# Performance work log

Hardware: AMD Instinct MI355X
Metric: run time of the kernel (lower is better)

## Reference

```python
import jax, jax.numpy as jnp
import numpy as np

D_MODEL = 1024
D_STATE = 16
LN_EPS = 1e-5


def setup_inputs() -> dict:
    key = jax.random.key(0)
    ks = jax.random.split(key, 10)
    B, T = 8, 4096
    s = 1.0 / np.sqrt(D_MODEL)
    inp = {
        "x": jax.random.normal(ks[0], (B, T, D_MODEL), jnp.float32),
        "h0": jnp.zeros((B, D_STATE), jnp.float32),
        "mask": jnp.ones((B, T), jnp.float32),
        # params
        "A_diag": -jnp.abs(jax.random.normal(ks[1], (D_STATE,), jnp.float32) * 0.01),
        "W_delta": jax.random.uniform(ks[2], (D_STATE, D_MODEL), jnp.float32, -s, s),
        "W_B": jax.random.uniform(ks[3], (D_STATE, D_MODEL), jnp.float32, -s, s),
        "W_C": jax.random.uniform(ks[4], (D_STATE, D_MODEL), jnp.float32, -s, s),
        "W_out": jax.random.uniform(ks[5], (D_MODEL, D_STATE), jnp.float32, -1/np.sqrt(D_STATE), 1/np.sqrt(D_STATE)),
        "D": jnp.ones((D_MODEL,), jnp.float32),
        "W_gate": jax.random.uniform(ks[6], (D_MODEL, D_MODEL), jnp.float32, -s, s),
        "b_gate": jax.random.uniform(ks[7], (D_MODEL,), jnp.float32, -s, s),
        "ln_w": jnp.ones((D_MODEL,), jnp.float32),
        "ln_b": jnp.zeros((D_MODEL,), jnp.float32),
    }
    return inp


def _layernorm(x, w, b):
    mu = jnp.mean(x, axis=-1, keepdims=True)
    var = jnp.var(x, axis=-1, keepdims=True)
    return (x - mu) * jax.lax.rsqrt(var + LN_EPS) * w + b


def reference(x, h0, mask, A_diag, W_delta, W_B, W_C, W_out, D, W_gate, b_gate, ln_w, ln_b):
    # Per-step projections depend only on x_t -> vectorize over T up front.
    gate = jax.nn.sigmoid(_layernorm(jnp.einsum('btd,ed->bte', x, W_gate) + b_gate, ln_w, ln_b))
    xg = gate * x                                        # [B,T,d_model]
    delta = jax.nn.softplus(jnp.einsum('btd,sd->bts', xg, W_delta))
    Bt = jnp.einsum('btd,sd->bts', xg, W_B)              # [B,T,d_state]
    Ct = jnp.einsum('btd,sd->bts', xg, W_C)
    A_bar = jnp.exp(delta * A_diag)                      # [B,T,d_state]
    m = mask[..., None]                                  # [B,T,1]

    def step(h, inputs):
        a_t, b_t, m_t = inputs                           # [B,ds],[B,ds],[B,1]
        h_cand = jnp.tanh(a_t * h + b_t)
        h_new = h_cand * m_t + h * (1.0 - m_t)
        return h_new, h_new

    # scan over time: move T to leading axis
    h_final, hs = jax.lax.scan(
        step, h0,
        (jnp.swapaxes(A_bar, 0, 1), jnp.swapaxes(Bt, 0, 1), jnp.swapaxes(m, 0, 1)))
    hs = jnp.swapaxes(hs, 0, 1)                          # [B,T,d_state]
    s = Ct * hs
    y = jnp.einsum('bts,ds->btd', s, W_out) + D * x      # [B,T,d_model]
    return (y, h_final)
```

## Files before the change

### kernel.cpp

```cpp
#include <hip/hip_runtime.h>
#include <hip/hip_bf16.h>
#include <cstdint>

#define M_TOK   32768
#define LNEPS   1e-5f
#define TWO_LOG2E 2.8853900817779268f

typedef float  f32x4 __attribute__((ext_vector_type(4)));
typedef short  s16x8 __attribute__((ext_vector_type(8)));
typedef unsigned long long ull;

__device__ __forceinline__ unsigned short f2b(float v) {
  return __builtin_bit_cast(unsigned short, __float2bfloat16(v));
}
__device__ __forceinline__ float b2f(unsigned short u) {
  return __bfloat162float(__builtin_bit_cast(__hip_bfloat16, u));
}
__device__ __forceinline__ float red64(float v) {
#pragma unroll
  for (int off = 32; off >= 1; off >>= 1) v += __shfl_xor(v, off, 64);
  return v;
}

__device__ __forceinline__ void async_cp16(const void* g, void* l) {
  using gp = const __attribute__((address_space(1))) char*;
  using lp = __attribute__((address_space(3))) char*;
  __builtin_amdgcn_global_load_lds((gp)(uint64_t)g,
                                   (lp)(uint32_t)(uint64_t)l, 16, 0, 0);
}

__global__ __launch_bounds__(256) void k_convert(
    const float* __restrict__ x, const float* __restrict__ wg,
    const float* __restrict__ wd, const float* __restrict__ wb,
    const float* __restrict__ wc,
    unsigned short* __restrict__ Xb, unsigned short* __restrict__ Wgb,
    unsigned short* __restrict__ Wcat) {
  int i = blockIdx.x * 256 + threadIdx.x;
  const float* src;
  unsigned short* dst;
  if (i < 8388608) {
    src = x + (size_t)i * 4; dst = Xb + (size_t)i * 4;
  } else if (i < 8650752) {
    int j = i - 8388608;
    src = wg + (size_t)j * 4; dst = Wgb + (size_t)j * 4;
  } else {
    int j = i - 8650752;
    int e = j * 4;
    if (e < 16384)       src = wd + e;
    else if (e < 32768)  src = wb + (e - 16384);
    else                 src = wc + (e - 32768);
    dst = Wcat + e;
  }
  float4 v = *(const float4*)src;
  ushort4 o;
  o.x = f2b(v.x); o.y = f2b(v.y); o.z = f2b(v.z); o.w = f2b(v.w);
  *(ushort4*)dst = o;
}

__global__ __launch_bounds__(256, 2) void k_gemm_gate(
    const unsigned short* __restrict__ A,
    const unsigned short* __restrict__ Bm,
    unsigned short* __restrict__ C) {
  __shared__ unsigned short As[128 * 32];
  __shared__ unsigned short Bs[128 * 32];
  const int tid  = threadIdx.x;
  const int wave = tid >> 6, lane = tid & 63;
  const int wr = wave >> 1, wc = wave & 1;
  const int lrow = lane & 15, lq = lane >> 4;
  const int lin  = blockIdx.y * gridDim.x + blockIdx.x;
  const int unit = (lin & 7) * 256 + (lin >> 3);
  const int m0 = (unit >> 3) * 128;
  const int n0 = (unit & 7) * 128;
  const int crow  = tid >> 2;
  const int ccol  = (tid & 3) * 8;

  f32x4 acc[4][4];
#pragma unroll
  for (int i = 0; i < 4; i++)
#pragma unroll
    for (int j = 0; j < 4; j++) acc[i][j] = (f32x4){0.f, 0.f, 0.f, 0.f};

  for (int k0 = 0; k0 < 1024; k0 += 32) {
    async_cp16(A + (size_t)(m0 + crow) * 1024 + k0 + ccol,
               (void*)(As + (wave * 64) * 8));
    async_cp16(A + (size_t)(m0 + crow + 64) * 1024 + k0 + ccol,
               (void*)(As + (256 + wave * 64) * 8));
    async_cp16(Bm + (size_t)(n0 + crow) * 1024 + k0 + ccol,
               (void*)(Bs + (wave * 64) * 8));
    async_cp16(Bm + (size_t)(n0 + crow + 64) * 1024 + k0 + ccol,
               (void*)(Bs + (256 + wave * 64) * 8));
    __syncthreads();

    s16x8 af[4], bfr[4];
#pragma unroll
    for (int i = 0; i < 4; i++)
      af[i] = *(const s16x8*)(As + (wr * 64 + i * 16 + lrow) * 32 + lq * 8);
#pragma unroll
    for (int j = 0; j < 4; j++)
      bfr[j] = *(const s16x8*)(Bs + (wc * 64 + j * 16 + lrow) * 32 + lq * 8);
#pragma unroll
    for (int i = 0; i < 4; i++)
#pragma unroll
      for (int j = 0; j < 4; j++)
        acc[i][j] = __builtin_amdgcn_mfma_f32_16x16x32_bf16(
            af[i], bfr[j], acc[i][j], 0, 0, 0);
    __syncthreads();
  }

#pragma unroll
  for (int i = 0; i < 4; i++)
#pragma unroll
    for (int j = 0; j < 4; j++)
#pragma unroll
      for (int r = 0; r < 4; r++) {
        int row = m0 + wr * 64 + i * 16 + lq * 4 + r;
        int col = n0 + wc * 64 + j * 16 + lrow;
        C[(size_t)row * 1024 + col] = f2b(acc[i][j][r]);
      }
}

__global__ __launch_bounds__(256) void k_lnproj(
    const unsigned short* __restrict__ G,
    const float* __restrict__ x,
    const float* __restrict__ bgp, const float* __restrict__ lnw,
    const float* __restrict__ lnb,
    const unsigned short* __restrict__ Wcat,
    const float* __restrict__ A_diag,
    float* __restrict__ UV, float* __restrict__ Ct, int* __restrict__ flags) {
  __shared__ unsigned short As[64 * 32];
  __shared__ unsigned short Bs[48 * 32];
  __shared__ float muL[64], rsL[64];
  const int tid  = threadIdx.x;
  const int wave = tid >> 6, lane = tid & 63;
  const int lrow = lane & 15, lq = lane >> 4;
  const int r0 = blockIdx.x * 64;
  const int crow = tid >> 2, ccol = (tid & 3) * 8;

  if (blockIdx.x == 0 && tid < 8)
    __hip_atomic_store(&flags[tid], 0, __ATOMIC_RELAXED,
                       __HIP_MEMORY_SCOPE_AGENT);

  {
    float bga[8], bgb[8];
    *(float4*)&bga[0] = *(const float4*)(bgp + lane * 8);
    *(float4*)&bga[4] = *(const float4*)(bgp + lane * 8 + 4);
    *(float4*)&bgb[0] = *(const float4*)(bgp + 512 + lane * 8);
    *(float4*)&bgb[4] = *(const float4*)(bgp + 512 + lane * 8 + 4);
    for (int rr = 0; rr < 16; ++rr) {
      const int row = wave * 16 + rr;
      const unsigned short* gp = G + (size_t)(r0 + row) * 1024;
      s16x8 ga = *(const s16x8*)(gp + lane * 8);
      s16x8 gb = *(const s16x8*)(gp + 512 + lane * 8);
      float s = 0.f, ss = 0.f;
#pragma unroll
      for (int i = 0; i < 8; i++) {
        float va = b2f((unsigned short)ga[i]) + bga[i];
        float vb = b2f((unsigned short)gb[i]) + bgb[i];
        s  += va + vb;
        ss += va * va + vb * vb;
      }
      s = red64(s); ss = red64(ss);
      if (lane == 0) {
        float mu  = s * (1.0f / 1024.0f);
        float var = ss * (1.0f / 1024.0f) - mu * mu;
        muL[row] = mu;
        rsL[row] = rsqrtf(var + LNEPS);
      }
    }
  }
  __syncthreads();
  const float mu = muL[crow];
  const float rs = rsL[crow];

  f32x4 acc[3];
#pragma unroll
  for (int j = 0; j < 3; j++) acc[j] = (f32x4){0.f, 0.f, 0.f, 0.f};

  for (int k0 = 0; k0 < 1024; k0 += 32) {
    s16x8 gv = *(const s16x8*)(G + (size_t)(r0 + crow) * 1024 + k0 + ccol);
    float xs[8], bgs[8], lws[8], lbs[8];
    *(float4*)&xs[0]  = *(const float4*)(x   + (size_t)(r0 + crow) * 1024 + k0 + ccol);
    *(float4*)&xs[4]  = *(const float4*)(x   + (size_t)(r0 + crow) * 1024 + k0 + ccol + 4);
    *(float4*)&bgs[0] = *(const float4*)(bgp + k0 + ccol);
    *(float4*)&bgs[4] = *(const float4*)(bgp + k0 + ccol + 4);
    *(float4*)&lws[0] = *(const float4*)(lnw + k0 + ccol);
    *(float4*)&lws[4] = *(const float4*)(lnw + k0 + ccol + 4);
    *(float4*)&lbs[0] = *(const float4*)(lnb + k0 + ccol);
    *(float4*)&lbs[4] = *(const float4*)(lnb + k0 + ccol + 4);
    uint4 bv;
    if (tid < 192) bv = *(const uint4*)(Wcat + (size_t)crow * 1024 + k0 + ccol);
    __syncthreads();
    s16x8 ov;
#pragma unroll
    for (int i = 0; i < 8; i++) {
      float v = b2f((unsigned short)gv[i]) + bgs[i];
      float u = (v - mu) * rs * lws[i] + lbs[i];
      float g = 1.0f / (1.0f + __expf(-u));
      ov[i] = (short)f2b(g * xs[i]);
    }
    *(s16x8*)(As + crow * 32 + ccol) = ov;
    if (tid < 192) *(uint4*)(Bs + crow * 32 + ccol) = bv;
    __syncthreads();
    s16x8 af = *(const s16x8*)(As + (wave * 16 + lrow) * 32 + lq * 8);
#pragma unroll
    for (int j = 0; j < 3; j++) {
      s16x8 bf8 = *(const s16x8*)(Bs + (j * 16 + lrow) * 32 + lq * 8);
      acc[j] = __builtin_amdgcn_mfma_f32_16x16x32_bf16(af, bf8, acc[j], 0, 0, 0);
    }
  }

  float ad = A_diag[lrow];
#pragma unroll
  for (int r = 0; r < 4; r++) {
    int row = r0 + wave * 16 + lq * 4 + r;
    float z  = acc[0][r];
    float sp = fmaxf(z, 0.0f) + log1pf(__expf(-fabsf(z)));
    float A2 = __expf(sp * ad) * TWO_LOG2E;
    float B2 = acc[1][r] * TWO_LOG2E;
    float2 o;
    o.x = A2 + B2;
    o.y = -2.0f * A2;
    *(float2*)(UV + (size_t)row * 32 + lrow * 2) = o;
    Ct[(size_t)row * 16 + lrow] = acc[2][r];
  }
}

#define TC 128
#define NCH (4096 / TC)
#define NOUT 512

__device__ __forceinline__ void load16(float2 (&P)[16], const float* uvb,
                                       int j, int lane) {
#pragma unroll
  for (int i = 0; i < 16; ++i)
    P[i] = *(const float2*)(uvb + ((j * 16 + i) * 16 + lane) * 2);
}
__device__ __forceinline__ void fast16(float2 (&P)[16], float& r, float& h,
                                       float* hhb, int j, int lane) {
#pragma unroll
  for (int i = 0; i < 16; ++i) {
    float w = fmaf(P[i].y, r, P[i].x);
    float e = __builtin_amdgcn_exp2f(w);
    r = __builtin_amdgcn_rcpf(e + 1.0f);
    h = fmaf(-2.0f, r, 1.0f);
    hhb[(j * 16 + i) * 16 + lane] = h;
  }
}
__device__ __forceinline__ void slow16(float2 (&P)[16], float& h,
                                       const float* mb, float* hhb,
                                       int j, int lane) {
#pragma unroll
  for (int i = 0; i < 16; ++i) {
    float v  = P[i].y, u = P[i].x;
    float A2 = -0.5f * v;
    float B2 = fmaf(0.5f, v, u);
    float w  = fmaf(A2, h, B2);
    float e  = __builtin_amdgcn_exp2f(w);
    float rr = __builtin_amdgcn_rcpf(e + 1.0f);
    float th = fmaf(-2.0f, rr, 1.0f);
    float m  = mb[j * 16 + i];
    h = fmaf(m, th - h, h);
    hhb[(j * 16 + i) * 16 + lane] = h;
  }
}

__global__ __launch_bounds__(512, 6) void k_scan_out(
    const float* __restrict__ UV, const float* __restrict__ mask,
    const float* __restrict__ h0, float* __restrict__ hs,
    float* __restrict__ hfin,
    const float* __restrict__ Ct, const float* __restrict__ x,
    const float* __restrict__ Wout, const float* __restrict__ Dd,
    float* __restrict__ y, int* __restrict__ flags) {
  __shared__ float uvL[2][TC * 32];
  __shared__ float hhL[2][TC * 16];
  __shared__ float mskL[2][TC];

  const int tid = threadIdx.x;

  if (blockIdx.x >= 8) {
    const int o    = blockIdx.x - 8;
    const int wv   = tid >> 6;
    const int lane = tid & 63;
    const int d0   = wv * 128 + lane * 2;
    const int b0   = o >> 7;
    const int b1   = b0 + 4;
    const int j0   = o & 127;

    float wa[16], wb[16];
#pragma unroll
    for (int q = 0; q < 4; q++) {
      *(float4*)&wa[q * 4] = *(const float4*)(Wout + (size_t)d0 * 16 + q * 4);
      *(float4*)&wb[q * 4] = *(const float4*)(Wout + (size_t)(d0 + 1) * 16 + q * 4);
    }
    float2 D2 = *(const float2*)(Dd + d0);

    for (int c = 0; c < NCH; ++c) {
      size_t r0 = (size_t)b0 * 4096 + (size_t)c * TC + j0;
      size_t r1 = (size_t)b1 * 4096 + (size_t)c * TC + j0;
      int spins = 0;
      for (;;) {
        int f = 0;
        if (lane == 0) {
          int fa = __hip_atomic_load(&flags[b0], __ATOMIC_RELAXED,
                                     __HIP_MEMORY_SCOPE_AGENT);
          int fb = __hip_atomic_load(&flags[b1], __ATOMIC_RELAXED,
                                     __HIP_MEMORY_SCOPE_AGENT);
          f = (fa < fb) ? fa : fb;
        }
        f = __shfl(f, 0);
        if (f > c || spins > (1 << 18)) break;
        ++spins;
        __builtin_amdgcn_s_sleep(32);
      }
      float cv0 = Ct[r0 * 16 + (lane & 15)];
      float cv1 = Ct[r1 * 16 + (lane & 15)];
      float hv0 = __hip_atomic_load(&hs[r0 * 16 + (lane & 15)],
                                    __ATOMIC_RELAXED, __HIP_MEMORY_SCOPE_AGENT);
      float hv1 = __hip_atomic_load(&hs[r1 * 16 + (lane & 15)],
                                    __ATOMIC_RELAXED, __HIP_MEMORY_SCOPE_AGENT);
      float2 x20 = *(const float2*)(x + r0 * 1024 + d0);
      float2 x21 = *(const float2*)(x + r1 * 1024 + d0);
      float sv0 = cv0 * hv0;
      float sv1 = cv1 * hv1;
      float a0x = D2.x * x20.x, a0y = D2.y * x20.y;
      float a1x = D2.x * x21.x, a1y = D2.y * x21.y;
#pragma unroll
      for (int s = 0; s < 16; s++) {
        float s0 = __shfl(sv0, s);
        float s1 = __shfl(sv1, s);
        a0x = fmaf(wa[s], s0, a0x);
        a0y = fmaf(wb[s], s0, a0y);
        a1x = fmaf(wa[s], s1, a1x);
        a1y = fmaf(wb[s], s1, a1y);
      }
      float2 o0; o0.x = a0x; o0.y = a0y;
      float2 o1; o1.x = a1x; o1.y = a1y;
      *(float2*)(y + r0 * 1024 + d0) = o0;
      *(float2*)(y + r1 * 1024 + d0) = o1;
    }
    return;
  }

  const int b   = blockIdx.x;
  const float* pm = mask + (size_t)b * 4096;
  const size_t uvbase = (size_t)b * 4096 * 32;
  const size_t hsbase = (size_t)b * 4096 * 16;

  if (tid < 64) __builtin_amdgcn_s_setprio(3);

  float h = 0.f, r = 0.f;
  if (tid < 16) {
    h = h0[b * 16 + tid];
    r = 0.5f - 0.5f * h;
  }

  if (tid >= 64) {
    int pt = tid - 64;
    const uint4* src = (const uint4*)(UV + uvbase);
    for (int i = pt; i < TC * 8; i += 448) ((uint4*)uvL[0])[i] = src[i];
    if (tid < 128) {
      int l = tid - 64;
      mskL[0][l]      = pm[l];
      mskL[0][l + 64] = pm[l + 64];
    }
  }
  __syncthreads();

  for (int c = 0; c < NCH; ++c) {
    if (c >= 2 && tid == 511) {
      __hip_atomic_store(&flags[b], c - 1, __ATOMIC_RELAXED,
                         __HIP_MEMORY_SCOPE_AGENT);
    }
    const int p = c & 1;
    if (tid < 64) {
      const int lane = tid;
      float mv0 = mskL[p][2 * lane], mv1 = mskL[p][2 * lane + 1];
      bool on = (mv0 == 1.0f) && (mv1 == 1.0f);
      bool allones = (__ballot(on) == 0xFFFFFFFFFFFFFFFFull);
      if (lane < 16) {
        const float* uvb = uvL[p];
        float* hhb = hhL[p];
        float2 Pa[16], Pb[16];
        load16(Pa, uvb, 0, lane);
        if (allones) {
#pragma unroll
          for (int j = 0; j < 8; j += 2) {
            load16(Pb, uvb, j + 1, lane);
            fast16(Pa, r, h, hhb, j, lane);
            if (j + 2 < 8) load16(Pa, uvb, j + 2, lane);
            fast16(Pb, r, h, hhb, j + 1, lane);
          }
        } else {
#pragma unroll
          for (int j = 0; j < 8; j += 2) {
            load16(Pb, uvb, j + 1, lane);
            slow16(Pa, h, mskL[p], hhb, j, lane);
            if (j + 2 < 8) load16(Pa, uvb, j + 2, lane);
            slow16(Pb, h, mskL[p], hhb, j + 1, lane);
          }
          r = 0.5f - 0.5f * h;
        }
      }
    } else {
      int pt = tid - 64;
      if (c + 1 < NCH) {
        const uint4* src =
            (const uint4*)(UV + uvbase + (size_t)(c + 1) * TC * 32);
        uint4* dst = (uint4*)uvL[(c + 1) & 1];
        for (int i = pt; i < TC * 8; i += 448) dst[i] = src[i];
        if (tid < 128) {
          int l = tid - 64;
          mskL[(c + 1) & 1][l]      = pm[(c + 1) * TC + l];
          mskL[(c + 1) & 1][l + 64] = pm[(c + 1) * TC + l + 64];
        }
      }
      if (c > 0) {
        const ull* s2 = (const ull*)hhL[(c - 1) & 1];
        ull* d2 = (ull*)(hs + hsbase + (size_t)(c - 1) * TC * 16);
        for (int i = pt; i < TC * 8; i += 448)
          __hip_atomic_store(&d2[i], s2[i], __ATOMIC_RELAXED,
                             __HIP_MEMORY_SCOPE_AGENT);
      }
    }
    __syncthreads();
  }

  {
    const ull* s2 = (const ull*)hhL[(NCH - 1) & 1];
    ull* d2 = (ull*)(hs + hsbase + (size_t)(NCH - 1) * TC * 16);
    for (int i = tid; i < TC * 8; i += 512)
      __hip_atomic_store(&d2[i], s2[i], __ATOMIC_RELAXED,
                         __HIP_MEMORY_SCOPE_AGENT);
  }
  __syncthreads();
  if (tid == 511) {
    __hip_atomic_store(&flags[b], NCH, __ATOMIC_RELAXED,
                       __HIP_MEMORY_SCOPE_AGENT);
  }
  if (tid < 16) hfin[b * 16 + tid] = h;
}

extern "C" void kernel_launch(void* const* d_in, const int* in_sizes, int n_in,
                              void* d_out, int out_size, void* d_ws, size_t ws_size,
                              hipStream_t stream) {
  const float* x       = (const float*)d_in[0];
  const float* h0      = (const float*)d_in[1];
  const float* mask    = (const float*)d_in[2];
  const float* A_diag  = (const float*)d_in[3];
  const float* W_delta = (const float*)d_in[4];
  const float* W_B     = (const float*)d_in[5];
  const float* W_C     = (const float*)d_in[6];
  const float* W_out   = (const float*)d_in[7];
  const float* Dd      = (const float*)d_in[8];
  const float* W_gate  = (const float*)d_in[9];
  const float* b_gate  = (const float*)d_in[10];
  const float* ln_w    = (const float*)d_in[11];
  const float* ln_b    = (const float*)d_in[12];

  char* ws = (char*)d_ws;
  unsigned short* Xb   = (unsigned short*)(ws);
  unsigned short* Gb   = (unsigned short*)(ws + 67108864);
  unsigned short* Wgb  = (unsigned short*)(ws + 134217728);
  unsigned short* Wcat = (unsigned short*)(ws + 136314880);
  int* flags = (int*)(ws + 136413184);
  float* UVb = (float*)(ws + 136445952);
  float* Ctb = (float*)(ws + 140640256);
  float* hsb = (float*)(ws + 142737408);

  float* y    = (float*)d_out;
  float* hfin = y + 33554432;

  hipLaunchKernelGGL(k_convert, dim3(33840), dim3(256), 0, stream,
                     x, W_gate, W_delta, W_B, W_C, Xb, Wgb, Wcat);
  hipLaunchKernelGGL(k_gemm_gate, dim3(256, 8), dim3(256), 0, stream, Xb, Wgb, Gb);
  hipLaunchKernelGGL(k_lnproj, dim3(512), dim3(256), 0, stream,
                     Gb, x, b_gate, ln_w, ln_b, Wcat, A_diag, UVb, Ctb, flags);
  hipLaunchKernelGGL(k_scan_out, dim3(8 + NOUT), dim3(512), 0, stream,
                     UVb, mask, h0, hsb, hfin, Ctb, x, W_out, Dd, y, flags);
}
```

Measured before the change: 497.9 us.

## Fuse LayerNorm row statistics into gate GEMM epilogue via atomics

The gate GEMM epilogue now adds the bias, reduces per-row sum and sum-of-squares across its tile and accumulates them into a global stats buffer with atomics. The conversion kernel zeroes that buffer. The LN+projection kernel then reads precomputed stats instead of re-reading the full gate output row to compute mean and variance, and is retiled to 32 rows per 128-thread block. This removes a full extra pass over G in the lnproj kernel, at the cost of atomic traffic, reuse of the hs buffer for stats, and statistics computed from fp32 accumulators rather than rounded bf16 values.

```diff
diff --git a/kernel.cpp b/kernel.cpp
--- a/kernel.cpp
+++ b/kernel.cpp
@@ -34,8 +34,12 @@
     const float* __restrict__ wd, const float* __restrict__ wb,
     const float* __restrict__ wc,
     unsigned short* __restrict__ Xb, unsigned short* __restrict__ Wgb,
-    unsigned short* __restrict__ Wcat) {
+    unsigned short* __restrict__ Wcat, float4* __restrict__ st4) {
   int i = blockIdx.x * 256 + threadIdx.x;
+  if (i >= 8663040) {
+    st4[i - 8663040] = (float4){0.f, 0.f, 0.f, 0.f};
+    return;
+  }
   const float* src;
   unsigned short* dst;
   if (i < 8388608) {
@@ -60,7 +64,8 @@
 __global__ __launch_bounds__(256, 2) void k_gemm_gate(
     const unsigned short* __restrict__ A,
     const unsigned short* __restrict__ Bm,
-    unsigned short* __restrict__ C) {
+    unsigned short* __restrict__ C,
+    const float* __restrict__ bg, float2* __restrict__ st) {
   __shared__ unsigned short As[128 * 32];
   __shared__ unsigned short Bs[128 * 32];
   const int tid  = threadIdx.x;
@@ -117,60 +122,57 @@
         int col = n0 + wc * 64 + j * 16 + lrow;
         C[(size_t)row * 1024 + col] = f2b(acc[i][j][r]);
       }
-}
-
-__global__ __launch_bounds__(256) void k_lnproj(
+
+  float bgj[4];
+#pragma unroll
+  for (int j = 0; j < 4; j++) bgj[j] = bg[n0 + wc * 64 + j * 16 + lrow];
+#pragma unroll
+  for (int i = 0; i < 4; i++)
+#pragma unroll
+    for (int r = 0; r < 4; r++) {
+      float sv = 0.f, sq = 0.f;
+#pragma unroll
+      for (int j = 0; j < 4; j++) {
+        float v = acc[i][j][r] + bgj[j];
+        sv += v; sq = fmaf(v, v, sq);
+      }
+#pragma unroll
+      for (int off = 1; off <= 8; off <<= 1) {
+        sv += __shfl_xor(sv, off, 64);
+        sq += __shfl_xor(sq, off, 64);
+      }
+      if (lrow == 0) {
+        int row = m0 + wr * 64 + i * 16 + lq * 4 + r;
+        atomicAdd(&st[row].x, sv);
+        atomicAdd(&st[row].y, sq);
+      }
+    }
+}
+
+__global__ __launch_bounds__(128) void k_lnproj(
     const unsigned short* __restrict__ G,
     const float* __restrict__ x,
     const float* __restrict__ bgp, const float* __restrict__ lnw,
     const float* __restrict__ lnb,
     const unsigned short* __restrict__ Wcat,
-    const float* __restrict__ A_diag,
+    const float* __restrict__ A_diag, const float2* __restrict__ st,
     float* __restrict__ UV, float* __restrict__ Ct, int* __restrict__ flags) {
-  __shared__ unsigned short As[64 * 32];
+  __shared__ unsigned short As[32 * 32];
   __shared__ unsigned short Bs[48 * 32];
-  __shared__ float muL[64], rsL[64];
   const int tid  = threadIdx.x;
   const int wave = tid >> 6, lane = tid & 63;
   const int lrow = lane & 15, lq = lane >> 4;
-  const int r0 = blockIdx.x * 64;
+  const int r0 = blockIdx.x * 32;
   const int crow = tid >> 2, ccol = (tid & 3) * 8;
 
   if (blockIdx.x == 0 && tid < 8)
     __hip_atomic_store(&flags[tid], 0, __ATOMIC_RELAXED,
                        __HIP_MEMORY_SCOPE_AGENT);
 
-  {
-    float bga[8], bgb[8];
-    *(float4*)&bga[0] = *(const float4*)(bgp + lane * 8);
-    *(float4*)&bga[4] = *(const float4*)(bgp + lane * 8 + 4);
-    *(float4*)&bgb[0] = *(const float4*)(bgp + 512 + lane * 8);
-    *(float4*)&bgb[4] = *(const float4*)(bgp + 512 + lane * 8 + 4);
-    for (int rr = 0; rr < 16; ++rr) {
-      const int row = wave * 16 + rr;
-      const unsigned short* gp = G + (size_t)(r0 + row) * 1024;
-      s16x8 ga = *(const s16x8*)(gp + lane * 8);
-      s16x8 gb = *(const s16x8*)(gp + 512 + lane * 8);
-      float s = 0.f, ss = 0.f;
-#pragma unroll
-      for (int i = 0; i < 8; i++) {
-        float va = b2f((unsigned short)ga[i]) + bga[i];
-        float vb = b2f((unsigned short)gb[i]) + bgb[i];
-        s  += va + vb;
-        ss += va * va + vb * vb;
-      }
-      s = red64(s); ss = red64(ss);
-      if (lane == 0) {
-        float mu  = s * (1.0f / 1024.0f);
-        float var = ss * (1.0f / 1024.0f) - mu * mu;
-        muL[row] = mu;
-        rsL[row] = rsqrtf(var + LNEPS);
-      }
-    }
-  }
-  __syncthreads();
-  const float mu = muL[crow];
-  const float rs = rsL[crow];
+  float2 s2 = st[r0 + crow];
+  const float mu = s2.x * (1.0f / 1024.0f);
+  const float var = s2.y * (1.0f / 1024.0f) - mu * mu;
+  const float rs = rsqrtf(var + LNEPS);
 
   f32x4 acc[3];
 #pragma unroll
@@ -187,8 +189,10 @@
     *(float4*)&lws[4] = *(const float4*)(lnw + k0 + ccol + 4);
     *(float4*)&lbs[0] = *(const float4*)(lnb + k0 + ccol);
     *(float4*)&lbs[4] = *(const float4*)(lnb + k0 + ccol + 4);
-    uint4 bv;
-    if (tid < 192) bv = *(const uint4*)(Wcat + (size_t)crow * 1024 + k0 + ccol);
+    uint4 bv0 = *(const uint4*)(Wcat + (size_t)crow * 1024 + k0 + ccol);
+    uint4 bv1;
+    if (tid < 64)
+      bv1 = *(const uint4*)(Wcat + (size_t)(32 + (tid >> 2)) * 1024 + k0 + ccol);
     __syncthreads();
     s16x8 ov;
 #pragma unroll
@@ -199,7 +203,8 @@
       ov[i] = (short)f2b(g * xs[i]);
     }
     *(s16x8*)(As + crow * 32 + ccol) = ov;
-    if (tid < 192) *(uint4*)(Bs + crow * 32 + ccol) = bv;
+    *(uint4*)(Bs + crow * 32 + ccol) = bv0;
+    if (tid < 64) *(uint4*)(Bs + (32 + (tid >> 2)) * 32 + ccol) = bv1;
     __syncthreads();
     s16x8 af = *(const s16x8*)(As + (wave * 16 + lrow) * 32 + lq * 8);
 #pragma unroll
@@ -466,15 +471,19 @@
   float* UVb = (float*)(ws + 136445952);
   float* Ctb = (float*)(ws + 140640256);
   float* hsb = (float*)(ws + 142737408);
+  float2* stats = (float2*)hsb;
 
   float* y    = (float*)d_out;
   float* hfin = y + 33554432;
 
-  hipLaunchKernelGGL(k_convert, dim3(33840), dim3(256), 0, stream,
-                     x, W_gate, W_delta, W_B, W_C, Xb, Wgb, Wcat);
-  hipLaunchKernelGGL(k_gemm_gate, dim3(256, 8), dim3(256), 0, stream, Xb, Wgb, Gb);
-  hipLaunchKernelGGL(k_lnproj, dim3(512), dim3(256), 0, stream,
-                     Gb, x, b_gate, ln_w, ln_b, Wcat, A_diag, UVb, Ctb, flags);
+  hipLaunchKernelGGL(k_convert, dim3(33904), dim3(256), 0, stream,
+                     x, W_gate, W_delta, W_B, W_C, Xb, Wgb, Wcat,
+                     (float4*)stats);
+  hipLaunchKernelGGL(k_gemm_gate, dim3(256, 8), dim3(256), 0, stream,
+                     Xb, Wgb, Gb, b_gate, stats);
+  hipLaunchKernelGGL(k_lnproj, dim3(1024), dim3(128), 0, stream,
+                     Gb, x, b_gate, ln_w, ln_b, Wcat, A_diag, stats,
+                     UVb, Ctb, flags);
   hipLaunchKernelGGL(k_scan_out, dim3(8 + NOUT), dim3(512), 0, stream,
                      UVb, mask, h0, hsb, hfin, Ctb, x, W_out, Dd, y, flags);
 }
```

Result: slower. 567.2 us (+13.9%).
